# Kernel optimization log

Hardware: AMD Instinct MI355X
Metric: run time of the kernel (lower is better)

## Reference

```python
import jax, jax.numpy as jnp
import numpy as np

EPS_NORM = 1e-5   # instance-norm epsilon (NormalizeLayer over spatial axes)
EPS_VAR = 1e-9    # floor used before sqrt, as in the original


def _instance_norm(x):
    # normalize over spatial axes (1,2), per batch & channel
    mean = jnp.mean(x, axis=(1, 2), keepdims=True)
    var = jnp.var(x, axis=(1, 2), keepdims=True)
    return (x - mean) * jax.lax.rsqrt(var + EPS_NORM)


def _aat(content, style, comb_c, comb_s):
    # content/style: (B,H,W,C); comb_*: (B,H,W,Cc)
    B, H, W, C = content.shape
    N = H * W
    norm_content = _instance_norm(content)
    q = _instance_norm(comb_c).reshape(B, N, -1)   # (B,N,Cc)
    k = _instance_norm(comb_s).reshape(B, N, -1)   # (B,N,Cc)
    v = style.reshape(B, N, C)                     # (B,N,C)
    scores = jnp.einsum('bnc,bmc->bnm', q, k)      # Q_T @ K
    A = jax.nn.softmax(scores, axis=-1)            # (B,N,N)
    M = jnp.einsum('bnm,bmc->bnc', A, v)           # weighted mean
    S2 = jnp.einsum('bnm,bmc->bnc', A, v * v) - M * M  # weighted variance
    S = jnp.sqrt(jnp.maximum(jax.nn.relu(S2), EPS_VAR))
    S = S.reshape(B, H, W, C)
    M = M.reshape(B, H, W, C)
    return S * norm_content + M


def _feature_loss(cs, c, s, cc, sc):
    aat = _aat(c, s, cc, sc)
    return jnp.mean(jnp.square(cs - aat))


def setup_inputs() -> dict:
    key = jax.random.key(0)
    shapes = {
        'cs2': (4, 64, 64, 256), 'c2': (4, 64, 64, 256), 's2': (4, 64, 64, 256),
        'cc2': (4, 64, 64, 448), 'sc2': (4, 64, 64, 448),
        'cs3': (4, 32, 32, 512), 'c3': (4, 32, 32, 512), 's3': (4, 32, 32, 512),
        'cc3': (4, 32, 32, 960), 'sc3': (4, 32, 32, 960),
        'cs4': (4, 16, 16, 512), 'c4': (4, 16, 16, 512), 's4': (4, 16, 16, 512),
        'cc4': (4, 16, 16, 1472), 'sc4': (4, 16, 16, 1472),
    }
    keys = jax.random.split(key, len(shapes))
    return {name: jax.random.normal(k, shp, dtype=jnp.float32)
            for k, (name, shp) in zip(keys, shapes.items())}


def reference(cs2, c2, s2, cc2, sc2, cs3, c3, s3, cc3, sc3, cs4, c4, s4, cc4, sc4):
    loss = _feature_loss(cs2, c2, s2, cc2, sc2)
    loss = loss + _feature_loss(cs3, c3, s3, cc3, sc3)
    loss = loss + _feature_loss(cs4, c4, s4, cc4, sc4)
    return loss
```

## Files before the change

### kernel.cpp

```cpp
#include <hip/hip_runtime.h>
#include <math.h>

#define EPS_NORM 1e-5f
#define EPS_VAR  1e-9f
#define LOG2E    1.4426950408889634f

typedef unsigned short ushort_t;
typedef __attribute__((ext_vector_type(4))) float f32x4;
typedef _Float16 half8 __attribute__((ext_vector_type(8)));

#define MFMAH(a, b, c) __builtin_amdgcn_mfma_f32_16x16x32_f16((a), (b), (c), 0, 0, 0)

#define GLD16(gp, lp) __builtin_amdgcn_global_load_lds(                          \
    (const __attribute__((address_space(1))) unsigned int*)(gp),                 \
    (__attribute__((address_space(3))) unsigned int*)(lp), 16, 0, 0)

__device__ inline ushort_t f16_bits(float x) {
    _Float16 h = (_Float16)x;
    ushort_t u;
    __builtin_memcpy(&u, &h, 2);
    return u;
}
__device__ inline half8 ldh(const ushort_t* p) {
    half8 h;
    __builtin_memcpy(&h, p, 16);
    return h;
}
__device__ inline uint4 pack8(const ushort_t* s) {
    uint4 r;
    r.x = (unsigned)s[0] | ((unsigned)s[1] << 16);
    r.y = (unsigned)s[2] | ((unsigned)s[3] << 16);
    r.z = (unsigned)s[4] | ((unsigned)s[5] << 16);
    r.w = (unsigned)s[6] | ((unsigned)s[7] << 16);
    return r;
}

struct StatJobs {
    const float* x[9];
    float* sm[9];
    float* sq[9];
    int N[9], Cn[9], chG[9], nG[9], base[9];
};
__global__ void __launch_bounds__(256) stat_partial_all(StatJobs J)
{
    int bx = blockIdx.x;
    int j = 0;
#pragma unroll
    for (int k = 1; k < 9; ++k) if (bx >= J.base[k]) j = k;
    bx -= J.base[j];
    const int N = J.N[j], Cn = J.Cn[j], chG = J.chG[j], nG = J.nG[j];
    int b  = bx / (chG * nG);
    int r  = bx % (chG * nG);
    int cg = r / nG;
    int ng = r % nG;
    int ch = cg * 256 + threadIdx.x;
    if (ch >= Cn) return;
    int n0 = ng * 256;
    int n1 = min(n0 + 256, N);
    const float* p = J.x[j] + (long)(b * N) * Cn + ch;
    float s = 0.f, ss = 0.f;
    for (int n = n0; n < n1; ++n) {
        float v = p[(long)n * Cn];
        s += v;
        ss = fmaf(v, v, ss);
    }
    atomicAdd(&J.sm[j][b * Cn + ch], s);
    atomicAdd(&J.sq[j][b * Cn + ch], ss);
}

struct FinJobs {
    float* sm[9];
    float* sq[9];
    int base[9];
    float invN[9];
    int total;
};
__global__ void __launch_bounds__(256) stat_finalize_all(FinJobs J)
{
    int i = blockIdx.x * 256 + threadIdx.x;
    if (i >= J.total) return;
    int j = 0;
#pragma unroll
    for (int k = 1; k < 9; ++k) if (i >= J.base[k]) j = k;
    int e = i - J.base[j];
    float m = J.sm[j][e] * J.invN[j];
    float v = J.sq[j][e] * J.invN[j] - m * m;
    J.sm[j][e] = m;
    J.sq[j][e] = rsqrtf(v + EPS_NORM);
}

struct PrepJobs {
    const float* qx[3]; const float* qm[3]; const float* qr[3]; ushort_t* qh[3];
    const float* kx[3]; const float* km[3]; const float* kr[3]; ushort_t* kh[3];
    const float* vx[3]; ushort_t* vt[3];
    int N[3], Cc[3], C[3], nbase[3];
};
__global__ void __launch_bounds__(256) prep_all(PrepJobs J)
{
    __shared__ __align__(16) ushort_t tbuf[64 * 72];
    int bx = blockIdx.x;
    int j = 0;
#pragma unroll
    for (int k = 1; k < 3; ++k) if (bx >= J.nbase[k]) j = k;
    bx -= J.nbase[j];
    const int N = J.N[j], Cc = J.Cc[j];
    const int normBlocks = 2 * N;
    if (bx < normBlocks) {
        const int wave = threadIdx.x >> 6, lane = threadIdx.x & 63;
        int rr = bx * 4 + wave;
        const int BN = 4 * N;
        const bool isQ = rr < BN;
        int bn = isQ ? rr : rr - BN;
        const float* x    = isQ ? J.qx[j] : J.kx[j];
        const float* mean = isQ ? J.qm[j] : J.km[j];
        const float* rstd = isQ ? J.qr[j] : J.kr[j];
        ushort_t* out     = isQ ? J.qh[j] : J.kh[j];
        const float scl   = isQ ? LOG2E : 1.0f;
        int b = bn / N;
        long base = (long)bn * Cc;
        const float* mb = mean + b * Cc;
        const float* rb = rstd + b * Cc;
        for (int c8 = lane; c8 * 8 < Cc; c8 += 64) {
            int ch = c8 * 8;
            float4 a0 = *(const float4*)(x + base + ch);
            float4 a1 = *(const float4*)(x + base + ch + 4);
            float4 m0 = *(const float4*)(mb + ch);
            float4 m1 = *(const float4*)(mb + ch + 4);
            float4 r0 = *(const float4*)(rb + ch);
            float4 r1 = *(const float4*)(rb + ch + 4);
            ushort_t h8[8];
            h8[0] = f16_bits((a0.x - m0.x) * r0.x * scl);
            h8[1] = f16_bits((a0.y - m0.y) * r0.y * scl);
            h8[2] = f16_bits((a0.z - m0.z) * r0.z * scl);
            h8[3] = f16_bits((a0.w - m0.w) * r0.w * scl);
            h8[4] = f16_bits((a1.x - m1.x) * r1.x * scl);
            h8[5] = f16_bits((a1.y - m1.y) * r1.y * scl);
            h8[6] = f16_bits((a1.z - m1.z) * r1.z * scl);
            h8[7] = f16_bits((a1.w - m1.w) * r1.w * scl);
            *(uint4*)(out + base + ch) = pack8(h8);
        }
    } else {
        int bid2 = bx - normBlocks;
        const int C = J.C[j];
        const int cT = C >> 6, nT = N >> 6;
        int b   = bid2 / (cT * nT);
        int rem = bid2 % (cT * nT);
        int ch0 = (rem / nT) << 6;
        int n0  = (rem % nT) << 6;
        const int lane = threadIdx.x & 63, wv = threadIdx.x >> 6;
        const float* vb_ = J.vx[j] + (long)b * N * C + ch0 + lane;
#pragma unroll
        for (int jj = 0; jj < 2; ++jj) {
            int nl = wv * 16 + jj * 8;
            ushort_t h8[8];
#pragma unroll
            for (int i = 0; i < 8; ++i)
                h8[i] = f16_bits(vb_[(long)(n0 + nl + i) * C]);
            *(uint4*)&tbuf[lane * 72 + nl] = pack8(h8);
        }
        __syncthreads();
        {
            const int chl = threadIdx.x >> 2;
            const int nq  = (threadIdx.x & 3) * 16;
            ushort_t* op = J.vt[j] + ((long)b * C + ch0 + chl) * N + n0 + nq;
            *(uint4*)op       = *(const uint4*)&tbuf[chl * 72 + nq];
            *(uint4*)(op + 8) = *(const uint4*)&tbuf[chl * 72 + nq + 8];
        }
    }
}

__device__ inline void stage64_async(const ushort_t* __restrict__ g, long rowBase,
                                     int gstride, int col0, ushort_t* slab, int tid)
{
    const int l  = tid & 63, w = tid >> 6;
    const int rs = l >> 3;
    const int cg = (l & 7) ^ rs;
#pragma unroll
    for (int i = 0; i < 2; ++i) {
        const int r = w * 16 + i * 8 + rs;
        const ushort_t* gp = g + (rowBase + r) * (long)gstride + col0 + (cg << 3);
        ushort_t* lp = slab + (w * 16 + i * 8) * 64 + l * 8;
        GLD16(gp, lp);
    }
}
template<int BROWS>
__device__ inline void stageQ_async(const ushort_t* __restrict__ g, long rowBase,
                                    int gstride, int col0, ushort_t* slab, int tid)
{
    if (tid < BROWS * 8) {
        const int l  = tid & 63, w = tid >> 6;
        const int rs = l >> 3;
        const int cg = (l & 7) ^ rs;
        const int r  = w * 8 + rs;
        const ushort_t* gp = g + (rowBase + r) * (long)gstride + col0 + (cg << 3);
        ushort_t* lp = slab + w * 8 * 64 + l * 8;
        GLD16(gp, lp);
    }
}
__device__ inline half8 ldsw(const ushort_t* slab, int row, int soff)
{
    const int gr = (soff >> 3) ^ (row & 7);
    return ldh(slab + row * 64 + (gr << 3));
}

__global__ void __launch_bounds__(256, 2) flash_pipe(
    const ushort_t* __restrict__ Qh, const ushort_t* __restrict__ Kh,
    const ushort_t* __restrict__ Vth,
    float* __restrict__ Pmo, float* __restrict__ Plo,
    float* __restrict__ PMo, float* __restrict__ PSo)
{
    constexpr int Cc = 448, C = 256, N = 4096, SPLIT = 2;
    constexpr int NKT  = (N / 64) / SPLIT;
    constexpr long VCHO = 64L * N;
    constexpr long KADV = 64L * Cc;

    __shared__ __align__(16) ushort_t smem[4 * 8192 + 4 * 1152];
    const int tid  = threadIdx.x;
    const int lane = tid & 63;
    const int w    = tid >> 6;
    const int l15  = lane & 15;
    const int quad = lane >> 4;

    const int grp = blockIdx.x & 7;
    const int sp  = grp & 1;
    const int b   = grp >> 1;
    const int qb  = (int)(blockIdx.x >> 3);
    const int i0 = qb * 64 + w * 16;
    const long po = (long)(b * (N / 16) + qb * 4 + w) * SPLIT + sp;

    const int rs    = lane >> 3;
    const int cg    = (lane & 7) ^ rs;
    const int ldso0 = w * 1024 + lane * 8;
    const int ldso1 = ldso0 + 512;
    const int xh    = l15 & 7;
    const int lb0   = l15 * 64 + ((quad)     ^ xh) * 8;
    const int lb1   = l15 * 64 + ((4 + quad) ^ xh) * 8;
    ushort_t* const Pw  = smem + 32768 + w * 1152;
    ushort_t* const pww = Pw + quad * 288 + l15;
    const ushort_t* const pfr = Pw + l15 * 72 + quad * 8;

    const long krow0 = (long)b * N + (long)sp * NKT * 64;
    const ushort_t* kp0 = Kh + (krow0 + w * 16 + rs) * (long)Cc + (cg << 3);
    const ushort_t* kp1 = kp0 + 8 * Cc;
    const ushort_t* vp0 = Vth + ((long)b * C + w * 16 + rs) * (long)N
                              + (cg << 3) + (long)sp * NKT * 64;
    const ushort_t* vp1 = vp0 + 8 * (long)N;

#define SLOT(k) (smem + (k) * 8192)
#define STGKP(c0, c1, slot, toff) do {                                           \
    GLD16(kp0 + (toff) + (c0) * 64, SLOT(slot) + ldso0);                         \
    GLD16(kp1 + (toff) + (c0) * 64, SLOT(slot) + ldso1);                         \
    GLD16(kp0 + (toff) + (c1) * 64, SLOT(slot) + 4096 + ldso0);                  \
    GLD16(kp1 + (toff) + (c1) * 64, SLOT(slot) + 4096 + ldso1); } while (0)
#define STGK1(c0, slot, toff) do {                                               \
    GLD16(kp0 + (toff) + (c0) * 64, SLOT(slot) + ldso0);                         \
    GLD16(kp1 + (toff) + (c0) * 64, SLOT(slot) + ldso1); } while (0)
#define STGVP(j0, slot, voff) do {                                               \
    GLD16(vp0 + (voff) + (j0) * VCHO, SLOT(slot) + ldso0);                       \
    GLD16(vp1 + (voff) + (j0) * VCHO, SLOT(slot) + ldso1);                       \
    GLD16(vp0 + (voff) + ((j0) + 1) * VCHO, SLOT(slot) + 4096 + ldso0);          \
    GLD16(vp1 + (voff) + ((j0) + 1) * VCHO, SLOT(slot) + 4096 + ldso1); } while (0)

#define WAITV(NN) asm volatile("s_waitcnt vmcnt(" #NN ")" ::: "memory");         \
    __builtin_amdgcn_sched_barrier(0);                                           \
    __builtin_amdgcn_s_barrier();                                                \
    __builtin_amdgcn_s_setprio(1);
#define PH_END __builtin_amdgcn_s_setprio(0);

#define QKPAIR(slot, c0) do {                                                    \
    const ushort_t* s0_ = SLOT(slot);                                            \
    const ushort_t* s1_ = s0_ + 4096;                                            \
    _Pragma("unroll")                                                            \
    for (int ct = 0; ct < 4; ++ct) S[ct] = MFMAH(qf[2*(c0)+0], ldh(s0_ + ct*1024 + lb0), S[ct]); \
    _Pragma("unroll")                                                            \
    for (int ct = 0; ct < 4; ++ct) S[ct] = MFMAH(qf[2*(c0)+1], ldh(s0_ + ct*1024 + lb1), S[ct]); \
    _Pragma("unroll")                                                            \
    for (int ct = 0; ct < 4; ++ct) S[ct] = MFMAH(qf[2*(c0)+2], ldh(s1_ + ct*1024 + lb0), S[ct]); \
    _Pragma("unroll")                                                            \
    for (int ct = 0; ct < 4; ++ct) S[ct] = MFMAH(qf[2*(c0)+3], ldh(s1_ + ct*1024 + lb1), S[ct]); } while (0)
#define QK1(slot, c0) do {                                                       \
    const ushort_t* s0_ = SLOT(slot);                                            \
    _Pragma("unroll")                                                            \
    for (int ct = 0; ct < 4; ++ct) S[ct] = MFMAH(qf[2*(c0)+0], ldh(s0_ + ct*1024 + lb0), S[ct]); \
    _Pragma("unroll")                                                            \
    for (int ct = 0; ct < 4; ++ct) S[ct] = MFMAH(qf[2*(c0)+1], ldh(s0_ + ct*1024 + lb1), S[ct]); } while (0)
#define PVPAIR(slot, ci0) do {                                                   \
    const ushort_t* s0_ = SLOT(slot);                                            \
    const ushort_t* s1_ = s0_ + 4096;                                            \
    _Pragma("unroll")                                                            \
    for (int ct = 0; ct < 4; ++ct) {                                             \
        half8 vh = ldh(s0_ + ct*1024 + lb0); half8 uh = vh * vh;                 \
        Mac[(ci0)*4 + ct] = MFMAH(pf0, vh, Mac[(ci0)*4 + ct]);                   \
        Sac[(ci0)*4 + ct] = MFMAH(pf0, uh, Sac[(ci0)*4 + ct]); }                 \
    _Pragma("unroll")                                                            \
    for (int ct = 0; ct < 4; ++ct) {                                             \
        half8 vh = ldh(s0_ + ct*1024 + lb1); half8 uh = vh * vh;                 \
        Mac[(ci0)*4 + ct] = MFMAH(pf1, vh, Mac[(ci0)*4 + ct]);                   \
        Sac[(ci0)*4 + ct] = MFMAH(pf1, uh, Sac[(ci0)*4 + ct]); }                 \
    _Pragma("unroll")                                                            \
    for (int ct = 0; ct < 4; ++ct) {                                             \
        half8 vh = ldh(s1_ + ct*1024 + lb0); half8 uh = vh * vh;                 \
        Mac[(ci0+1)*4 + ct] = MFMAH(pf0, vh, Mac[(ci0+1)*4 + ct]);               \
        Sac[(ci0+1)*4 + ct] = MFMAH(pf0, uh, Sac[(ci0+1)*4 + ct]); }             \
    _Pragma("unroll")                                                            \
    for (int ct = 0; ct < 4; ++ct) {                                             \
        half8 vh = ldh(s1_ + ct*1024 + lb1); half8 uh = vh * vh;                 \
        Mac[(ci0+1)*4 + ct] = MFMAH(pf1, vh, Mac[(ci0+1)*4 + ct]);               \
        Sac[(ci0+1)*4 + ct] = MFMAH(pf1, uh, Sac[(ci0+1)*4 + ct]); } } while (0)
#define RESET_S do {                                                             \
    _Pragma("unroll")                                                            \
    for (int ct = 0; ct < 4; ++ct)                                               \
        _Pragma("unroll")                                                        \
        for (int r = 0; r < 4; ++r) S[ct][r] = 0.f; } while (0)

    half8 qf[14];
    {
        const ushort_t* q1 = Qh + ((long)(b * N + i0 + l15)) * Cc + quad * 8;
#pragma unroll
        for (int ks = 0; ks < 14; ++ks) qf[ks] = ldh(q1 + ks * 32);
    }
    asm volatile("s_waitcnt vmcnt(0)" ::: "memory");

    float m_r[4], l_l[4], mw = -1e30f;
    f32x4 Mac[16], Sac[16];
    f32x4 S[4];
    half8 pf0, pf1;
#pragma unroll
    for (int r = 0; r < 4; ++r) { m_r[r] = -1e30f; l_l[r] = 0.f; }
#pragma unroll
    for (int ct = 0; ct < 16; ++ct)
#pragma unroll
        for (int r = 0; r < 4; ++r) { Mac[ct][r] = 0.f; Sac[ct][r] = 0.f; }

    auto softmax_step = [&]() {
        float tmax = S[0][0];
#pragma unroll
        for (int ct = 0; ct < 4; ++ct)
#pragma unroll
            for (int r = 0; r < 4; ++r) tmax = fmaxf(tmax, S[ct][r]);
#pragma unroll
        for (int off = 1; off <= 32; off <<= 1)
            tmax = fmaxf(tmax, __shfl_xor(tmax, off, 64));

        if (tmax > mw + 14.4269504f) {
            float rm[4];
#pragma unroll
            for (int r = 0; r < 4; ++r)
                rm[r] = fmaxf(fmaxf(S[0][r], S[1][r]), fmaxf(S[2][r], S[3][r]));
#pragma unroll
            for (int off = 1; off <= 8; off <<= 1)
#pragma unroll
                for (int r = 0; r < 4; ++r)
                    rm[r] = fmaxf(rm[r], __shfl_xor(rm[r], off, 64));
#pragma unroll
            for (int r = 0; r < 4; ++r) {
                float mn = fmaxf(m_r[r], rm[r]);
                float corr = exp2f(m_r[r] - mn);
                m_r[r] = mn;
                l_l[r] *= corr;
#pragma unroll
                for (int ct = 0; ct < 16; ++ct) { Mac[ct][r] *= corr; Sac[ct][r] *= corr; }
            }
            float tt = fminf(fminf(m_r[0], m_r[1]), fminf(m_r[2], m_r[3]));
            tt = fminf(tt, __shfl_xor(tt, 16, 64));
            tt = fminf(tt, __shfl_xor(tt, 32, 64));
            mw = tt;
        }
#pragma unroll
        for (int ct = 0; ct < 4; ++ct)
#pragma unroll
            for (int r = 0; r < 4; ++r) {
                float p = exp2f(S[ct][r] - m_r[r]);
                l_l[r] += p;
                pww[r * 72 + ct * 16] = f16_bits(p);
            }
        pf0 = ldh(pfr);
        pf1 = ldh(pfr + 32);
    };

    STGKP(0, 1, 0, 0);
    STGKP(2, 3, 1, 0);

    for (int it = 0; it < NKT / 2; ++it) {
        RESET_S;
        STGKP(4, 5, 2, 0);
        WAITV(8)  QKPAIR(0, 0); PH_END;
        STGK1(6, 3, 0);
        WAITV(6)  QKPAIR(1, 2); PH_END;
        STGVP(0, 0, 0);
        WAITV(6)  QKPAIR(2, 4); PH_END;
        STGVP(2, 1, 0);
        WAITV(8)  QK1(3, 6); PH_END;
        softmax_step();
        STGKP(0, 1, 2, KADV);
        WAITV(8)  PVPAIR(0, 0); PH_END;
        STGKP(2, 3, 3, KADV);
        WAITV(8)  PVPAIR(1, 2); PH_END;

        RESET_S;
        STGKP(4, 5, 0, KADV);
        WAITV(8)  QKPAIR(2, 0); PH_END;
        STGK1(6, 1, KADV);
        WAITV(6)  QKPAIR(3, 2); PH_END;
        STGVP(0, 2, 64);
        WAITV(6)  QKPAIR(0, 4); PH_END;
        STGVP(2, 3, 64);
        WAITV(8)  QK1(1, 6); PH_END;
        softmax_step();
        const bool more = (it + 1 < NKT / 2);
        if (more) {
            kp0 += 2 * KADV; kp1 += 2 * KADV;
            STGKP(0, 1, 0, 0);
            asm volatile("s_waitcnt vmcnt(8)" ::: "memory");
        } else {
            asm volatile("s_waitcnt vmcnt(4)" ::: "memory");
        }
        __builtin_amdgcn_sched_barrier(0);
        __builtin_amdgcn_s_barrier();
        __builtin_amdgcn_s_setprio(1);
        PVPAIR(2, 0);
        PH_END;
        if (more) {
            STGKP(2, 3, 1, 0);
            asm volatile("s_waitcnt vmcnt(8)" ::: "memory");
        } else {
            asm volatile("s_waitcnt vmcnt(0)" ::: "memory");
        }
        __builtin_amdgcn_sched_barrier(0);
        __builtin_amdgcn_s_barrier();
        __builtin_amdgcn_s_setprio(1);
        PVPAIR(3, 2);
        PH_END;

        vp0 += 128; vp1 += 128;
    }
#undef SLOT
#undef STGKP
#undef STGK1
#undef STGVP
#undef WAITV
#undef PH_END
#undef QKPAIR
#undef QK1
#undef PVPAIR
#undef RESET_S

#pragma unroll
    for (int off = 1; off <= 8; off <<= 1)
#pragma unroll
        for (int r = 0; r < 4; ++r) l_l[r] += __shfl_xor(l_l[r], off, 64);

    if (l15 == 0) {
#pragma unroll
        for (int r = 0; r < 4; ++r) {
            Pmo[po * 16 + quad * 4 + r] = m_r[r];
            Plo[po * 16 + quad * 4 + r] = l_l[r];
        }
    }
#pragma unroll
    for (int ct = 0; ct < 16; ++ct)
#pragma unroll
        for (int r = 0; r < 4; ++r) {
            long idx = (po * 16 + quad * 4 + r) * C + ct * 16 + l15;
            PMo[idx] = Mac[ct][r];
            PSo[idx] = Sac[ct][r];
        }
}

template<int Cc, int C, int N, int CSPLIT, bool QREG, int SPLIT, int SLABS, int KGRP>
__global__ void __launch_bounds__(256, 2) flash_mfma(
    const ushort_t* __restrict__ Qh, const ushort_t* __restrict__ Kh,
    const ushort_t* __restrict__ Vth,
    float* __restrict__ Pmo, float* __restrict__ Plo,
    float* __restrict__ PMo, float* __restrict__ PSo)
{
    constexpr int KC      = Cc / 64;
    constexpr int VC      = C / 64;
    constexpr int VCW     = VC / CSPLIT;
    constexpr int CTCW    = 4 * VCW;
    constexpr int STRIPES = 4 / CSPLIT;
    constexpr int BROWS   = 16 * STRIPES;
    constexpr int QB      = N / BROWS;
    constexpr int TILES   = N / 64;
    constexpr int NKT     = TILES / SPLIT;
    constexpr int NKS     = QREG ? (Cc / 32) : 1;
    constexpr int NGRP    = (KC + KGRP - 1) / KGRP;
    constexpr int G       = 4 / CSPLIT;
    constexpr int QCH     = BROWS * 64;
    constexpr int QOFF    = KGRP * 4096;
    constexpr int KQEND   = QOFF + KGRP * QCH;
    constexpr int REGION  = QREG ? (SLABS * 4096)
                                 : (KQEND > SLABS * 4096 ? KQEND : SLABS * 4096);

    __shared__ __align__(16) ushort_t smem[REGION + 4 * 1152];
    const int tid  = threadIdx.x;
    const int lane = tid & 63;
    const int w    = tid >> 6;
    const int l15  = lane & 15;
    const int quad = lane >> 4;

    const int bq = blockIdx.x / SPLIT;
    const int sp = blockIdx.x % SPLIT;
    const int b  = bq / QB;
    const int qb = bq % QB;
    const int ls  = w / CSPLIT;
    const int ch2 = w % CSPLIT;
    const int i0 = qb * BROWS + ls * 16;
    const long po = (long)(b * (N / 16) + qb * STRIPES + ls) * SPLIT + sp;
    ushort_t* Pw = smem + REGION + w * 1152;

    half8 qf[NKS];
    if constexpr (QREG) {
        const ushort_t* q1 = Qh + ((long)(b * N + i0 + l15)) * Cc + quad * 8;
#pragma unroll
        for (int ks = 0; ks < NKS; ++ks) qf[ks] = ldh(q1 + ks * 32);
    }

    float m_r[4], l_l[4], mw = -1e30f;
    f32x4 Mac[CTCW], Sac[CTCW];
#pragma unroll
    for (int r = 0; r < 4; ++r) { m_r[r] = -1e30f; l_l[r] = 0.f; }
#pragma unroll
    for (int ct = 0; ct < CTCW; ++ct)
#pragma unroll
        for (int r = 0; r < 4; ++r) { Mac[ct][r] = 0.f; Sac[ct][r] = 0.f; }

    for (int kt = sp * NKT; kt < sp * NKT + NKT; ++kt) {
        const long krow = (long)b * N + kt * 64;

        f32x4 S[4];
#pragma unroll
        for (int ct = 0; ct < 4; ++ct)
#pragma unroll
            for (int r = 0; r < 4; ++r) S[ct][r] = 0.f;

#pragma unroll
        for (int grp = 0; grp < NGRP; ++grp) {
            const int g0 = grp * KGRP;
            const int gn = (KC - g0 < KGRP) ? (KC - g0) : KGRP;
            __syncthreads();
#pragma unroll
            for (int j = 0; j < KGRP; ++j) if (j < gn) {
                stage64_async(Kh, krow, Cc, (g0 + j) * 64, smem + j * 4096, tid);
                if constexpr (!QREG)
                    stageQ_async<BROWS>(Qh, (long)b * N + qb * BROWS, Cc, (g0 + j) * 64,
                                        smem + QOFF + j * QCH, tid);
            }
            __syncthreads();
#pragma unroll
            for (int j = 0; j < KGRP; ++j) if (j < gn) {
#pragma unroll
                for (int ks = 0; ks < 2; ++ks) {
                    half8 a;
                    if constexpr (QREG) a = qf[(g0 + j) * 2 + ks];
                    else a = ldsw(smem + QOFF + j * QCH, ls * 16 + l15, ks * 32 + quad * 8);
#pragma unroll
                    for (int ct = 0; ct < 4; ++ct) {
                        half8 bf = ldsw(smem + j * 4096, ct * 16 + l15, ks * 32 + quad * 8);
                        S[ct] = MFMAH(a, bf, S[ct]);
                    }
                }
            }
        }

        float tmax = S[0][0];
#pragma unroll
        for (int ct = 0; ct < 4; ++ct)
#pragma unroll
            for (int r = 0; r < 4; ++r) tmax = fmaxf(tmax, S[ct][r]);
#pragma unroll
        for (int off = 1; off <= 32; off <<= 1)
            tmax = fmaxf(tmax, __shfl_xor(tmax, off, 64));

        if (tmax > mw + 14.4269504f) {
            float rm[4];
#pragma unroll
            for (int r = 0; r < 4; ++r)
                rm[r] = fmaxf(fmaxf(S[0][r], S[1][r]), fmaxf(S[2][r], S[3][r]));
#pragma unroll
            for (int off = 1; off <= 8; off <<= 1)
#pragma unroll
                for (int r = 0; r < 4; ++r)
                    rm[r] = fmaxf(rm[r], __shfl_xor(rm[r], off, 64));
#pragma unroll
            for (int r = 0; r < 4; ++r) {
                float mn = fmaxf(m_r[r], rm[r]);
                float corr = exp2f(m_r[r] - mn);
                m_r[r] = mn;
                l_l[r] *= corr;
#pragma unroll
                for (int ct = 0; ct < CTCW; ++ct) { Mac[ct][r] *= corr; Sac[ct][r] *= corr; }
            }
            float t = fminf(fminf(m_r[0], m_r[1]), fminf(m_r[2], m_r[3]));
            t = fminf(t, __shfl_xor(t, 16, 64));
            t = fminf(t, __shfl_xor(t, 32, 64));
            mw = t;
        }

#pragma unroll
        for (int ct = 0; ct < 4; ++ct)
#pragma unroll
            for (int r = 0; r < 4; ++r) {
                float p = exp2f(S[ct][r] - m_r[r]);
                l_l[r] += p;
                Pw[(quad * 4 + r) * 72 + ct * 16 + l15] = f16_bits(p);
            }

        half8 pf0 = ldh(Pw + l15 * 72 + 0  + quad * 8);
        half8 pf1 = ldh(Pw + l15 * 72 + 32 + quad * 8);

#pragma unroll
        for (int g = 0; g < VCW; g += G) {
            __syncthreads();
#pragma unroll
            for (int s = 0; s < 4; ++s) {
                const int h = s / G, j = s % G;
                stage64_async(Vth, (long)b * C + (h * VCW + g + j) * 64, N, kt * 64,
                              smem + s * 4096, tid);
            }
            __syncthreads();
#pragma unroll
            for (int ks = 0; ks < 2; ++ks) {
                half8 pf = ks ? pf1 : pf0;
#pragma unroll
                for (int j = 0; j < G; ++j)
#pragma unroll
                    for (int ct = 0; ct < 4; ++ct) {
                        half8 vh = ldsw(smem + (ch2 * G + j) * 4096,
                                        ct * 16 + l15, ks * 32 + quad * 8);
                        half8 uh = vh * vh;
                        const int ci = (g + j) * 4 + ct;
                        Mac[ci] = MFMAH(pf, vh, Mac[ci]);
                        Sac[ci] = MFMAH(pf, uh, Sac[ci]);
                    }
            }
        }
    }

#pragma unroll
    for (int off = 1; off <= 8; off <<= 1)
#pragma unroll
        for (int r = 0; r < 4; ++r) l_l[r] += __shfl_xor(l_l[r], off, 64);

    if (ch2 == 0 && l15 == 0) {
#pragma unroll
        for (int r = 0; r < 4; ++r) {
            Pmo[po * 16 + quad * 4 + r] = m_r[r];
            Plo[po * 16 + quad * 4 + r] = l_l[r];
        }
    }
    const int chb = ch2 * (C / CSPLIT);
#pragma unroll
    for (int ct = 0; ct < CTCW; ++ct)
#pragma unroll
        for (int r = 0; r < 4; ++r) {
            long idx = (po * 16 + quad * 4 + r) * C + chb + ct * 16 + l15;
            PMo[idx] = Mac[ct][r];
            PSo[idx] = Sac[ct][r];
        }
}

template<int C, int SPLIT>
__global__ void __launch_bounds__(256) combine_aat(
    const float* __restrict__ Pm, const float* __restrict__ Pl,
    const float* __restrict__ PM, const float* __restrict__ PS,
    const float* __restrict__ CT, const float* __restrict__ CS,
    const float* __restrict__ cmean, const float* __restrict__ crstd,
    float* __restrict__ loss, int N)
{
    constexpr int CL4 = C / 4;
    __shared__ float wS[SPLIT][16];
    __shared__ float invL[16];
    __shared__ float red[4];
    const int pi = blockIdx.x;
    const int nb = N / 16;
    const int b  = pi / nb;
    const long g0 = (long)b * N + (long)(pi % nb) * 16;
    const int tid = threadIdx.x;

    if (tid < 16) {
        float m = -1e30f;
#pragma unroll
        for (int s = 0; s < SPLIT; ++s)
            m = fmaxf(m, Pm[((long)pi * SPLIT + s) * 16 + tid]);
        float L = 0.f;
#pragma unroll
        for (int s = 0; s < SPLIT; ++s) {
            float e = exp2f(Pm[((long)pi * SPLIT + s) * 16 + tid] - m);
            wS[s][tid] = e;
            L = fmaf(e, Pl[((long)pi * SPLIT + s) * 16 + tid], L);
        }
        invL[tid] = 1.f / L;
    }
    __syncthreads();

    float acc = 0.f;
    for (int v = tid; v < 4 * C; v += 256) {
        const int r  = v / CL4;
        const int c0 = (v - r * CL4) * 4;
        const long q0 = (((long)pi * SPLIT) * 16 + r) * C + c0;
        float4 Ms = {0.f, 0.f, 0.f, 0.f}, Ss = {0.f, 0.f, 0.f, 0.f};
#pragma unroll
        for (int s = 0; s < SPLIT; ++s) {
            const float ws_ = wS[s][r];
            const float4 pm = *(const float4*)&PM[q0 + (long)s * 16 * C];
            const float4 ps = *(const float4*)&PS[q0 + (long)s * 16 * C];
            Ms.x = fmaf(ws_, pm.x, Ms.x); Ms.y = fmaf(ws_, pm.y, Ms.y);
            Ms.z = fmaf(ws_, pm.z, Ms.z); Ms.w = fmaf(ws_, pm.w, Ms.w);
            Ss.x = fmaf(ws_, ps.x, Ss.x); Ss.y = fmaf(ws_, ps.y, Ss.y);
            Ss.z = fmaf(ws_, ps.z, Ss.z); Ss.w = fmaf(ws_, ps.w, Ss.w);
        }
        const float iL = invL[r];
        const float4 ctv = *(const float4*)&CT[(g0 + r) * C + c0];
        const float4 csv = *(const float4*)&CS[(g0 + r) * C + c0];
        const float4 cmv = *(const float4*)&cmean[b * C + c0];
        const float4 crv = *(const float4*)&crstd[b * C + c0];
#pragma unroll
        for (int e = 0; e < 4; ++e) {
            const float Msx = (&Ms.x)[e] * iL;
            const float S2  = (&Ss.x)[e] * iL - Msx * Msx;
            const float Sx  = sqrtf(fmaxf(S2, EPS_VAR));
            const float nc  = ((&ctv.x)[e] - (&cmv.x)[e]) * (&crv.x)[e];
            const float d   = (&csv.x)[e] - (Sx * nc + Msx);
            acc = fmaf(d, d, acc);
        }
    }
#pragma unroll
    for (int off = 1; off <= 32; off <<= 1) acc += __shfl_xor(acc, off, 64);
    if ((tid & 63) == 0) red[tid >> 6] = acc;
    __syncthreads();
    if (tid == 0) atomicAdd(loss, red[0] + red[1] + red[2] + red[3]);
}

template<int CCL, int CL, int NQ>
__global__ void __launch_bounds__(256) flash_aat(
    const float* __restrict__ Q, const float* __restrict__ K, const float* __restrict__ V,
    const float* __restrict__ CT, const float* __restrict__ CS,
    const float* __restrict__ qmean, const float* __restrict__ qrstd,
    const float* __restrict__ kmean, const float* __restrict__ krstd,
    const float* __restrict__ cmean, const float* __restrict__ crstd,
    float* __restrict__ loss, int N)
{
    constexpr int CC   = CCL * 64;
    constexpr int C    = CL * 64;
    constexpr int ROWS = 4 * NQ;
    const int lane = threadIdx.x & 63;
    const int wave = threadIdx.x >> 6;
    const int rowBlocks = N / ROWS;
    const int b  = blockIdx.x / rowBlocks;
    const int rb = blockIdx.x % rowBlocks;
    const int i0 = rb * ROWS + wave * NQ;

    float kmu[CCL], krs[CCL];
#pragma unroll
    for (int t = 0; t < CCL; ++t) {
        int ch = lane + 64 * t;
        kmu[t] = kmean[b * CC + ch];
        krs[t] = krstd[b * CC + ch];
    }
    float q[NQ][CCL];
#pragma unroll
    for (int qi = 0; qi < NQ; ++qi) {
        long base = (long)(b * N + i0 + qi) * CC;
#pragma unroll
        for (int t = 0; t < CCL; ++t) {
            int ch = lane + 64 * t;
            q[qi][t] = (Q[base + ch] - qmean[b * CC + ch]) * qrstd[b * CC + ch];
        }
    }
    float mval[NQ], lsum[NQ];
    float Macc[NQ][CL], Sacc[NQ][CL];
#pragma unroll
    for (int qi = 0; qi < NQ; ++qi) {
        mval[qi] = -1e30f; lsum[qi] = 0.f;
#pragma unroll
        for (int t = 0; t < CL; ++t) { Macc[qi][t] = 0.f; Sacc[qi][t] = 0.f; }
    }
    for (int j = 0; j < N; ++j) {
        long kb = (long)(b * N + j) * CC;
        float dot[NQ];
#pragma unroll
        for (int qi = 0; qi < NQ; ++qi) dot[qi] = 0.f;
#pragma unroll
        for (int t = 0; t < CCL; ++t) {
            float kv = (K[kb + lane + 64 * t] - kmu[t]) * krs[t];
#pragma unroll
            for (int qi = 0; qi < NQ; ++qi) dot[qi] = fmaf(q[qi][t], kv, dot[qi]);
        }
#pragma unroll
        for (int off = 32; off > 0; off >>= 1)
#pragma unroll
            for (int qi = 0; qi < NQ; ++qi) dot[qi] += __shfl_xor(dot[qi], off, 64);
        long vb = (long)(b * N + j) * C;
        float vv[CL];
#pragma unroll
        for (int t = 0; t < CL; ++t) vv[t] = V[vb + lane + 64 * t];
#pragma unroll
        for (int qi = 0; qi < NQ; ++qi) {
            float s = dot[qi];
            float p;
            if (s > mval[qi]) {
                float cr2 = __expf(mval[qi] - s);
                lsum[qi] *= cr2;
#pragma unroll
                for (int t = 0; t < CL; ++t) { Macc[qi][t] *= cr2; Sacc[qi][t] *= cr2; }
                mval[qi] = s; p = 1.f;
            } else p = __expf(s - mval[qi]);
            lsum[qi] += p;
#pragma unroll
            for (int t = 0; t < CL; ++t) {
                float pv = p * vv[t];
                Macc[qi][t] += pv;
                Sacc[qi][t] = fmaf(pv, vv[t], Sacc[qi][t]);
            }
        }
    }
    float acc = 0.f;
#pragma unroll
    for (int qi = 0; qi < NQ; ++qi) {
        float inv_l = 1.f / lsum[qi];
        long base = (long)(b * N + i0 + qi) * C;
#pragma unroll
        for (int t = 0; t < CL; ++t) {
            int ch = lane + 64 * t;
            float M  = Macc[qi][t] * inv_l;
            float S2 = Sacc[qi][t] * inv_l - M * M;
            float S  = sqrtf(fmaxf(S2, EPS_VAR));
            float nc = (CT[base + ch] - cmean[b * C + ch]) * crstd[b * C + ch];
            float d  = CS[base + ch] - (S * nc + M);
            acc = fmaf(d, d, acc);
        }
    }
#pragma unroll
    for (int off = 32; off > 0; off >>= 1) acc += __shfl_xor(acc, off, 64);
    if (lane == 0) atomicAdd(loss, acc);
}

__global__ void combine_loss(const float* __restrict__ lp, float* __restrict__ out,
                             float s0, float s1, float s2)
{
    out[0] = lp[0] * s0 + lp[1] * s1 + lp[2] * s2;
}

extern "C" void kernel_launch(void* const* d_in, const int* in_sizes, int n_in,
                              void* d_out, int out_size, void* d_ws, size_t ws_size,
                              hipStream_t stream)
{
    const float* cs2 = (const float*)d_in[0];
    const float* c2  = (const float*)d_in[1];
    const float* s2v = (const float*)d_in[2];
    const float* cc2 = (const float*)d_in[3];
    const float* sc2 = (const float*)d_in[4];
    const float* cs3 = (const float*)d_in[5];
    const float* c3  = (const float*)d_in[6];
    const float* s3v = (const float*)d_in[7];
    const float* cc3 = (const float*)d_in[8];
    const float* sc3 = (const float*)d_in[9];
    const float* cs4 = (const float*)d_in[10];
    const float* c4  = (const float*)d_in[11];
    const float* s4v = (const float*)d_in[12];
    const float* cc4 = (const float*)d_in[13];
    const float* sc4 = (const float*)d_in[14];

    const int B = 4;
    float* ws = (float*)d_ws;
    size_t fo = 0;
    auto allocF = [&](size_t n) { float* p = ws + fo; fo += n; return p; };

    float* lossp = allocF(4);
    float* c2m = allocF(B * 256);  float* c2r = allocF(B * 256);
    float* q2m = allocF(B * 448);  float* q2r = allocF(B * 448);
    float* k2m = allocF(B * 448);  float* k2r = allocF(B * 448);
    float* c3m = allocF(B * 512);  float* c3r = allocF(B * 512);
    float* q3m = allocF(B * 960);  float* q3r = allocF(B * 960);
    float* k3m = allocF(B * 960);  float* k3r = allocF(B * 960);
    float* c4m = allocF(B * 512);  float* c4r = allocF(B * 512);
    float* q4m = allocF(B * 1472); float* q4r = allocF(B * 1472);
    float* k4m = allocF(B * 1472); float* k4r = allocF(B * 1472);
    size_t zeroBytes = fo * sizeof(float);

    float* Pm = allocF(32768);
    float* Pl = allocF(32768);
    float* PM = allocF(8388608);
    float* PS = allocF(8388608);

    size_t arenaOff = ((fo * 4 + 15) & ~(size_t)15) / 2;
    ushort_t* arena = (ushort_t*)d_ws + arenaOff;
    const size_t arenaShorts = 18874400;
    size_t need = arenaOff * 2 + arenaShorts * 2;
    const bool fast = (ws_size >= need);

    hipMemsetAsync(d_ws, 0, zeroBytes, stream);

    {
        StatJobs SJ; FinJobs FJ;
        const float* xs[9] = {c2, cc2, sc2, c3, cc3, sc3, c4, cc4, sc4};
        float* sms[9] = {c2m, q2m, k2m, c3m, q3m, k3m, c4m, q4m, k4m};
        float* sqs[9] = {c2r, q2r, k2r, c3r, q3r, k3r, c4r, q4r, k4r};
        const int Ns[9]  = {4096, 4096, 4096, 1024, 1024, 1024, 256, 256, 256};
        const int Cns[9] = {256, 448, 448, 512, 960, 960, 512, 1472, 1472};
        int pb = 0, fb = 0;
        for (int j = 0; j < 9; ++j) {
            int chG = (Cns[j] + 255) / 256;
            int nG  = (Ns[j] + 255) / 256;
            SJ.x[j] = xs[j]; SJ.sm[j] = sms[j]; SJ.sq[j] = sqs[j];
            SJ.N[j] = Ns[j]; SJ.Cn[j] = Cns[j]; SJ.chG[j] = chG; SJ.nG[j] = nG;
            SJ.base[j] = pb;
            pb += B * chG * nG;
            FJ.sm[j] = sms[j]; FJ.sq[j] = sqs[j]; FJ.base[j] = fb;
            FJ.invN[j] = 1.0f / (float)Ns[j];
            fb += B * Cns[j];
        }
        FJ.total = fb;
        hipLaunchKernelGGL(stat_partial_all, dim3(pb), dim3(256), 0, stream, SJ);
        hipLaunchKernelGGL(stat_finalize_all, dim3((fb + 255) / 256), dim3(256), 0, stream, FJ);
    }

    if (fast) {
        auto arenaFor = [&](size_t& o, size_t n) {
            ushort_t* p = arena + o; o += (n + 7) & ~(size_t)7; return p;
        };
        size_t o2 = 0;
        ushort_t* qh2 = arenaFor(o2, (size_t)B*4096*448);
        ushort_t* kh2 = arenaFor(o2, (size_t)B*4096*448);
        ushort_t* vh2 = arenaFor(o2, (size_t)B*4096*256);
        size_t o3 = 0;
        ushort_t* qh3 = arenaFor(o3, (size_t)B*1024*960);
        ushort_t* kh3 = arenaFor(o3, (size_t)B*1024*960);
        ushort_t* vh3 = arenaFor(o3, (size_t)B*1024*512);
        size_t o4 = 0;
        ushort_t* qh4 = arenaFor(o4, (size_t)B*256*1472);
        ushort_t* kh4 = arenaFor(o4, (size_t)B*256*1472);
        ushort_t* vh4 = arenaFor(o4, (size_t)B*256*512);

        const int vt2 = (256/64)*(4096/64)*B;
        const int vt3 = (512/64)*(1024/64)*B;
        const int vt4 = (512/64)*(256/64)*B;

        size_t totShorts = o2 + o3 + o4;
        bool prepFused = (ws_size >= arenaOff * 2 + totShorts * 2);
        if (prepFused) {
            qh3 = arena + o2;        kh3 = qh3 + (((size_t)B*1024*960 + 7) & ~(size_t)7);
            vh3 = kh3 + (((size_t)B*1024*960 + 7) & ~(size_t)7);
            qh4 = arena + o2 + o3;   kh4 = qh4 + (((size_t)B*256*1472 + 7) & ~(size_t)7);
            vh4 = kh4 + (((size_t)B*256*1472 + 7) & ~(size_t)7);

            PrepJobs PJ;
            PJ.qx[0]=cc2; PJ.qm[0]=q2m; PJ.qr[0]=q2r; PJ.qh[0]=qh2;
            PJ.kx[0]=sc2; PJ.km[0]=k2m; PJ.kr[0]=k2r; PJ.kh[0]=kh2;
            PJ.vx[0]=s2v; PJ.vt[0]=vh2; PJ.N[0]=4096; PJ.Cc[0]=448; PJ.C[0]=256;
            PJ.qx[1]=cc3; PJ.qm[1]=q3m; PJ.qr[1]=q3r; PJ.qh[1]=qh3;
            PJ.kx[1]=sc3; PJ.km[1]=k3m; PJ.kr[1]=k3r; PJ.kh[1]=kh3;
            PJ.vx[1]=s3v; PJ.vt[1]=vh3; PJ.N[1]=1024; PJ.Cc[1]=960; PJ.C[1]=512;
            PJ.qx[2]=cc4; PJ.qm[2]=q4m; PJ.qr[2]=q4r; PJ.qh[2]=qh4;
            PJ.kx[2]=sc4; PJ.km[2]=k4m; PJ.kr[2]=k4r; PJ.kh[2]=kh4;
            PJ.vx[2]=s4v; PJ.vt[2]=vh4; PJ.N[2]=256;  PJ.Cc[2]=1472; PJ.C[2]=512;
            int g0n = 2*4096 + vt2;
            int g1n = 2*1024 + vt3;
            int g2n = 2*256  + vt4;
            PJ.nbase[0] = 0; PJ.nbase[1] = g0n; PJ.nbase[2] = g0n + g1n;
            hipLaunchKernelGGL(prep_all, dim3(g0n + g1n + g2n), dim3(256), 0, stream, PJ);
        }

        {
            if (!prepFused) {
                PrepJobs PJ;
                PJ.qx[0]=cc2; PJ.qm[0]=q2m; PJ.qr[0]=q2r; PJ.qh[0]=qh2;
                PJ.kx[0]=sc2; PJ.km[0]=k2m; PJ.kr[0]=k2r; PJ.kh[0]=kh2;
                PJ.vx[0]=s2v; PJ.vt[0]=vh2; PJ.N[0]=4096; PJ.Cc[0]=448; PJ.C[0]=256;
                for (int k = 1; k < 3; ++k) { PJ.N[k]=4096; PJ.Cc[k]=448; PJ.C[k]=256;
                    PJ.qx[k]=cc2; PJ.qm[k]=q2m; PJ.qr[k]=q2r; PJ.qh[k]=qh2;
                    PJ.kx[k]=sc2; PJ.km[k]=k2m; PJ.kr[k]=k2r; PJ.kh[k]=kh2;
                    PJ.vx[k]=s2v; PJ.vt[k]=vh2; }
                int gn = 2*4096 + vt2;
                PJ.nbase[0]=0; PJ.nbase[1]=gn; PJ.nbase[2]=gn;
                hipLaunchKernelGGL(prep_all, dim3(gn), dim3(256), 0, stream, PJ);
            }
            hipLaunchKernelGGL(flash_pipe, dim3(B*(4096/64)*2), dim3(256), 0, stream,
                               qh2, kh2, vh2, Pm, Pl, PM, PS);
            hipLaunchKernelGGL((combine_aat<256, 2>), dim3(B*4096/16), dim3(256), 0, stream,
                               Pm, Pl, PM, PS, c2, cs2, c2m, c2r, &lossp[0], 4096);
        }
        {
            if (!prepFused) {
                PrepJobs PJ;
                PJ.qx[0]=cc3; PJ.qm[0]=q3m; PJ.qr[0]=q3r; PJ.qh[0]=qh3;
                PJ.kx[0]=sc3; PJ.km[0]=k3m; PJ.kr[0]=k3r; PJ.kh[0]=kh3;
                PJ.vx[0]=s3v; PJ.vt[0]=vh3; PJ.N[0]=1024; PJ.Cc[0]=960; PJ.C[0]=512;
                for (int k = 1; k < 3; ++k) { PJ.N[k]=1024; PJ.Cc[k]=960; PJ.C[k]=512;
                    PJ.qx[k]=cc3; PJ.qm[k]=q3m; PJ.qr[k]=q3r; PJ.qh[k]=qh3;
                    PJ.kx[k]=sc3; PJ.km[k]=k3m; PJ.kr[k]=k3r; PJ.kh[k]=kh3;
                    PJ.vx[k]=s3v; PJ.vt[k]=vh3; }
                int gn = 2*1024 + vt3;
                PJ.nbase[0]=0; PJ.nbase[1]=gn; PJ.nbase[2]=gn;
                hipLaunchKernelGGL(prep_all, dim3(gn), dim3(256), 0, stream, PJ);
            }
            hipLaunchKernelGGL((flash_mfma<960, 512, 1024, 2, false, 4, 5, 5>),
                               dim3(B*(1024/32)*4), dim3(256), 0, stream,
                               qh3, kh3, vh3, Pm, Pl, PM, PS);
            hipLaunchKernelGGL((combine_aat<512, 4>), dim3(B*1024/16), dim3(256), 0, stream,
                               Pm, Pl, PM, PS, c3, cs3, c3m, c3r, &lossp[1], 1024);
        }
        {
            if (!prepFused) {
                PrepJobs PJ;
                PJ.qx[0]=cc4; PJ.qm[0]=q4m; PJ.qr[0]=q4r; PJ.qh[0]=qh4;
                PJ.kx[0]=sc4; PJ.km[0]=k4m; PJ.kr[0]=k4r; PJ.kh[0]=kh4;
                PJ.vx[0]=s4v; PJ.vt[0]=vh4; PJ.N[0]=256; PJ.Cc[0]=1472; PJ.C[0]=512;
                for (int k = 1; k < 3; ++k) { PJ.N[k]=256; PJ.Cc[k]=1472; PJ.C[k]=512;
                    PJ.qx[k]=cc4; PJ.qm[k]=q4m; PJ.qr[k]=q4r; PJ.qh[k]=qh4;
                    PJ.kx[k]=sc4; PJ.km[k]=k4m; PJ.kr[k]=k4r; PJ.kh[k]=kh4;
                    PJ.vx[k]=s4v; PJ.vt[k]=vh4; }
                int gn = 2*256 + vt4;
                PJ.nbase[0]=0; PJ.nbase[1]=gn; PJ.nbase[2]=gn;
                hipLaunchKernelGGL(prep_all, dim3(gn), dim3(256), 0, stream, PJ);
            }
            hipLaunchKernelGGL((flash_mfma<1472, 512, 256, 4, false, 4, 6, 6>),
                               dim3(B*(256/16)*4), dim3(256), 0, stream,
                               qh4, kh4, vh4, Pm, Pl, PM, PS);
            hipLaunchKernelGGL((combine_aat<512, 4>), dim3(B*256/16), dim3(256), 0, stream,
                               Pm, Pl, PM, PS, c4, cs4, c4m, c4r, &lossp[2], 256);
        }
    } else {
        hipLaunchKernelGGL((flash_aat<7, 4, 4>), dim3(B * 4096 / 16), dim3(256), 0, stream,
                           cc2, sc2, s2v, c2, cs2, q2m, q2r, k2m, k2r, c2m, c2r, &lossp[0], 4096);
        hipLaunchKernelGGL((flash_aat<15, 8, 2>), dim3(B * 1024 / 8), dim3(256), 0, stream,
                           cc3, sc3, s3v, c3, cs3, q3m, q3r, k3m, k3r, c3m, c3r, &lossp[1], 1024);
        hipLaunchKernelGGL((flash_aat<23, 8, 2>), dim3(B * 256 / 8), dim3(256), 0, stream,
                           cc4, sc4, s4v, c4, cs4, q4m, q4r, k4m, k4r, c4m, c4r, &lossp[2], 256);
    }

    hipLaunchKernelGGL(combine_loss, dim3(1), dim3(1), 0, stream,
                       lossp, (float*)d_out,
                       1.0f / (4.0f * 4096.0f * 256.0f),
                       1.0f / (4.0f * 1024.0f * 512.0f),
                       1.0f / (4.0f * 256.0f * 512.0f));
}
```

Baseline: 682.1 us.

## Fuse level-3 and level-4 flash/combine launches and split QK^T across channel waves

Merges the level-3 and level-4 flash kernels into one grid, and likewise their combine kernels, so the smaller level-4 work fills the GPU alongside level 3 instead of running as a separate underfilled launch. Inside flash_body, waves that share a row stripe but handle different output-channel halves now each compute only a subset of the Cc chunks of Q·K^T and sum partial scores through shared memory, removing the redundant score MFMAs those waves used to repeat. Level-4 partials go to a separate workspace tail. The cost is two extra block barriers per key tile plus LDS traffic for the reduction, and a fixed shared-memory size across both instantiations.

```diff
diff --git a/kernel.cpp b/kernel.cpp
--- a/kernel.cpp
+++ b/kernel.cpp
@@ -468,11 +468,12 @@
 }
 
 template<int Cc, int C, int N, int CSPLIT, bool QREG, int SPLIT, int SLABS, int KGRP>
-__global__ void __launch_bounds__(256, 2) flash_mfma(
+__device__ __forceinline__ void flash_body(
     const ushort_t* __restrict__ Qh, const ushort_t* __restrict__ Kh,
     const ushort_t* __restrict__ Vth,
     float* __restrict__ Pmo, float* __restrict__ Plo,
-    float* __restrict__ PMo, float* __restrict__ PSo)
+    float* __restrict__ PMo, float* __restrict__ PSo,
+    ushort_t* smem, int bid)
 {
     constexpr int KC      = Cc / 64;
     constexpr int VC      = C / 64;
@@ -492,15 +493,14 @@
     constexpr int REGION  = QREG ? (SLABS * 4096)
                                  : (KQEND > SLABS * 4096 ? KQEND : SLABS * 4096);
 
-    __shared__ __align__(16) ushort_t smem[REGION + 4 * 1152];
     const int tid  = threadIdx.x;
     const int lane = tid & 63;
     const int w    = tid >> 6;
     const int l15  = lane & 15;
     const int quad = lane >> 4;
 
-    const int bq = blockIdx.x / SPLIT;
-    const int sp = blockIdx.x % SPLIT;
+    const int bq = bid / SPLIT;
+    const int sp = bid % SPLIT;
     const int b  = bq / QB;
     const int qb = bq % QB;
     const int ls  = w / CSPLIT;
@@ -549,16 +549,37 @@
             __syncthreads();
 #pragma unroll
             for (int j = 0; j < KGRP; ++j) if (j < gn) {
-#pragma unroll
-                for (int ks = 0; ks < 2; ++ks) {
-                    half8 a;
-                    if constexpr (QREG) a = qf[(g0 + j) * 2 + ks];
-                    else a = ldsw(smem + QOFF + j * QCH, ls * 16 + l15, ks * 32 + quad * 8);
-#pragma unroll
-                    for (int ct = 0; ct < 4; ++ct) {
-                        half8 bf = ldsw(smem + j * 4096, ct * 16 + l15, ks * 32 + quad * 8);
-                        S[ct] = MFMAH(a, bf, S[ct]);
+                if (((g0 + j) % CSPLIT) == ch2) {
+#pragma unroll
+                    for (int ks = 0; ks < 2; ++ks) {
+                        half8 a;
+                        if constexpr (QREG) a = qf[(g0 + j) * 2 + ks];
+                        else a = ldsw(smem + QOFF + j * QCH, ls * 16 + l15, ks * 32 + quad * 8);
+#pragma unroll
+                        for (int ct = 0; ct < 4; ++ct) {
+                            half8 bf = ldsw(smem + j * 4096, ct * 16 + l15, ks * 32 + quad * 8);
+                            S[ct] = MFMAH(a, bf, S[ct]);
+                        }
                     }
+                }
+            }
+        }
+
+        if constexpr (CSPLIT > 1) {
+            float* sred = (float*)smem;
+            __syncthreads();
+#pragma unroll
+            for (int ct = 0; ct < 4; ++ct)
+                *(f32x4*)&sred[(w * 4 + ct) * 256 + lane * 4] = S[ct];
+            __syncthreads();
+#pragma unroll
+            for (int p = 0; p < 4; ++p) {
+                if (p == w) continue;
+                if ((p / CSPLIT) != ls) continue;
+#pragma unroll
+                for (int ct = 0; ct < 4; ++ct) {
+                    f32x4 t = *(const f32x4*)&sred[(p * 4 + ct) * 256 + lane * 4];
+                    S[ct] = S[ct] + t;
                 }
             }
         }
@@ -660,19 +681,49 @@
         }
 }
 
+template<int Cc, int C, int N, int CSPLIT, bool QREG, int SPLIT, int SLABS, int KGRP>
+__global__ void __launch_bounds__(256, 2) flash_mfma(
+    const ushort_t* __restrict__ Qh, const ushort_t* __restrict__ Kh,
+    const ushort_t* __restrict__ Vth,
+    float* __restrict__ Pmo, float* __restrict__ Plo,
+    float* __restrict__ PMo, float* __restrict__ PSo)
+{
+    __shared__ __align__(16) ushort_t smem[35328];
+    flash_body<Cc, C, N, CSPLIT, QREG, SPLIT, SLABS, KGRP>(
+        Qh, Kh, Vth, Pmo, Plo, PMo, PSo, smem, (int)blockIdx.x);
+}
+
+__global__ void __launch_bounds__(256, 2) flash34(
+    const ushort_t* __restrict__ Qh3, const ushort_t* __restrict__ Kh3,
+    const ushort_t* __restrict__ Vth3,
+    float* __restrict__ Pm3, float* __restrict__ Pl3,
+    float* __restrict__ PM3, float* __restrict__ PS3,
+    const ushort_t* __restrict__ Qh4, const ushort_t* __restrict__ Kh4,
+    const ushort_t* __restrict__ Vth4,
+    float* __restrict__ Pm4, float* __restrict__ Pl4,
+    float* __restrict__ PM4, float* __restrict__ PS4, int G3)
+{
+    __shared__ __align__(16) ushort_t smem[35328];
+    if ((int)blockIdx.x < G3)
+        flash_body<960, 512, 1024, 2, false, 4, 5, 5>(
+            Qh3, Kh3, Vth3, Pm3, Pl3, PM3, PS3, smem, (int)blockIdx.x);
+    else
+        flash_body<1472, 512, 256, 4, false, 4, 6, 6>(
+            Qh4, Kh4, Vth4, Pm4, Pl4, PM4, PS4, smem, (int)blockIdx.x - G3);
+}
+
 template<int C, int SPLIT>
-__global__ void __launch_bounds__(256) combine_aat(
+__device__ __forceinline__ void combine_body(
     const float* __restrict__ Pm, const float* __restrict__ Pl,
     const float* __restrict__ PM, const float* __restrict__ PS,
     const float* __restrict__ CT, const float* __restrict__ CS,
     const float* __restrict__ cmean, const float* __restrict__ crstd,
-    float* __restrict__ loss, int N)
+    float* __restrict__ loss, int N, int pi, float* shm)
 {
     constexpr int CL4 = C / 4;
-    __shared__ float wS[SPLIT][16];
-    __shared__ float invL[16];
-    __shared__ float red[4];
-    const int pi = blockIdx.x;
+    float (*wS)[16] = (float(*)[16])shm;
+    float* invL = shm + SPLIT * 16;
+    float* red  = invL + 16;
     const int nb = N / 16;
     const int b  = pi / nb;
     const long g0 = (long)b * N + (long)(pi % nb) * 16;
@@ -730,6 +781,40 @@
     if ((tid & 63) == 0) red[tid >> 6] = acc;
     __syncthreads();
     if (tid == 0) atomicAdd(loss, red[0] + red[1] + red[2] + red[3]);
+}
+
+template<int C, int SPLIT>
+__global__ void __launch_bounds__(256) combine_aat(
+    const float* __restrict__ Pm, const float* __restrict__ Pl,
+    const float* __restrict__ PM, const float* __restrict__ PS,
+    const float* __restrict__ CT, const float* __restrict__ CS,
+    const float* __restrict__ cmean, const float* __restrict__ crstd,
+    float* __restrict__ loss, int N)
+{
+    __shared__ float shm[SPLIT * 16 + 20];
+    combine_body<C, SPLIT>(Pm, Pl, PM, PS, CT, CS, cmean, crstd, loss, N,
+                           (int)blockIdx.x, shm);
+}
+
+__global__ void __launch_bounds__(256) combine34(
+    const float* __restrict__ Pm3, const float* __restrict__ Pl3,
+    const float* __restrict__ PM3, const float* __restrict__ PS3,
+    const float* __restrict__ CT3, const float* __restrict__ CS3,
+    const float* __restrict__ cm3, const float* __restrict__ cr3,
+    float* __restrict__ l3, int N3,
+    const float* __restrict__ Pm4, const float* __restrict__ Pl4,
+    const float* __restrict__ PM4, const float* __restrict__ PS4,
+    const float* __restrict__ CT4, const float* __restrict__ CS4,
+    const float* __restrict__ cm4, const float* __restrict__ cr4,
+    float* __restrict__ l4, int N4, int G3)
+{
+    __shared__ float shm[4 * 16 + 20];
+    if ((int)blockIdx.x < G3)
+        combine_body<512, 4>(Pm3, Pl3, PM3, PS3, CT3, CS3, cm3, cr3, l3, N3,
+                             (int)blockIdx.x, shm);
+    else
+        combine_body<512, 4>(Pm4, Pl4, PM4, PS4, CT4, CS4, cm4, cr4, l4, N4,
+                             (int)blockIdx.x - G3, shm);
 }
 
 template<int CCL, int CL, int NQ>
@@ -939,6 +1024,16 @@
 
         size_t totShorts = o2 + o3 + o4;
         bool prepFused = (ws_size >= arenaOff * 2 + totShorts * 2);
+
+        const size_t PS4N = (size_t)256 * 16 * 512;
+        size_t tailByte = (((arenaOff + totShorts) * 2) + 255) & ~(size_t)255;
+        bool fused34 = prepFused && (ws_size >= tailByte + 2 * PS4N * 4);
+        float* PM4 = nullptr; float* PS4 = nullptr;
+        if (fused34) {
+            PM4 = (float*)((char*)d_ws + tailByte);
+            PS4 = PM4 + PS4N;
+        }
+
         if (prepFused) {
             qh3 = arena + o2;        kh3 = qh3 + (((size_t)B*1024*960 + 7) & ~(size_t)7);
             vh3 = kh3 + (((size_t)B*1024*960 + 7) & ~(size_t)7);
@@ -981,45 +1076,60 @@
             hipLaunchKernelGGL((combine_aat<256, 2>), dim3(B*4096/16), dim3(256), 0, stream,
                                Pm, Pl, PM, PS, c2, cs2, c2m, c2r, &lossp[0], 4096);
         }
-        {
-            if (!prepFused) {
-                PrepJobs PJ;
-                PJ.qx[0]=cc3; PJ.qm[0]=q3m; PJ.qr[0]=q3r; PJ.qh[0]=qh3;
-                PJ.kx[0]=sc3; PJ.km[0]=k3m; PJ.kr[0]=k3r; PJ.kh[0]=kh3;
-                PJ.vx[0]=s3v; PJ.vt[0]=vh3; PJ.N[0]=1024; PJ.Cc[0]=960; PJ.C[0]=512;
-                for (int k = 1; k < 3; ++k) { PJ.N[k]=1024; PJ.Cc[k]=960; PJ.C[k]=512;
-                    PJ.qx[k]=cc3; PJ.qm[k]=q3m; PJ.qr[k]=q3r; PJ.qh[k]=qh3;
-                    PJ.kx[k]=sc3; PJ.km[k]=k3m; PJ.kr[k]=k3r; PJ.kh[k]=kh3;
-                    PJ.vx[k]=s3v; PJ.vt[k]=vh3; }
-                int gn = 2*1024 + vt3;
-                PJ.nbase[0]=0; PJ.nbase[1]=gn; PJ.nbase[2]=gn;
-                hipLaunchKernelGGL(prep_all, dim3(gn), dim3(256), 0, stream, PJ);
-            }
-            hipLaunchKernelGGL((flash_mfma<960, 512, 1024, 2, false, 4, 5, 5>),
-                               dim3(B*(1024/32)*4), dim3(256), 0, stream,
-                               qh3, kh3, vh3, Pm, Pl, PM, PS);
-            hipLaunchKernelGGL((combine_aat<512, 4>), dim3(B*1024/16), dim3(256), 0, stream,
-                               Pm, Pl, PM, PS, c3, cs3, c3m, c3r, &lossp[1], 1024);
-        }
-        {
-            if (!prepFused) {
-                PrepJobs PJ;
-                PJ.qx[0]=cc4; PJ.qm[0]=q4m; PJ.qr[0]=q4r; PJ.qh[0]=qh4;
-                PJ.kx[0]=sc4; PJ.km[0]=k4m; PJ.kr[0]=k4r; PJ.kh[0]=kh4;
-                PJ.vx[0]=s4v; PJ.vt[0]=vh4; PJ.N[0]=256; PJ.Cc[0]=1472; PJ.C[0]=512;
-                for (int k = 1; k < 3; ++k) { PJ.N[k]=256; PJ.Cc[k]=1472; PJ.C[k]=512;
-                    PJ.qx[k]=cc4; PJ.qm[k]=q4m; PJ.qr[k]=q4r; PJ.qh[k]=qh4;
-                    PJ.kx[k]=sc4; PJ.km[k]=k4m; PJ.kr[k]=k4r; PJ.kh[k]=kh4;
-                    PJ.vx[k]=s4v; PJ.vt[k]=vh4; }
-                int gn = 2*256 + vt4;
-                PJ.nbase[0]=0; PJ.nbase[1]=gn; PJ.nbase[2]=gn;
-                hipLaunchKernelGGL(prep_all, dim3(gn), dim3(256), 0, stream, PJ);
-            }
-            hipLaunchKernelGGL((flash_mfma<1472, 512, 256, 4, false, 4, 6, 6>),
-                               dim3(B*(256/16)*4), dim3(256), 0, stream,
-                               qh4, kh4, vh4, Pm, Pl, PM, PS);
-            hipLaunchKernelGGL((combine_aat<512, 4>), dim3(B*256/16), dim3(256), 0, stream,
-                               Pm, Pl, PM, PS, c4, cs4, c4m, c4r, &lossp[2], 256);
+
+        if (fused34) {
+            const int G3 = B*(1024/32)*4;
+            const int G4 = B*(256/16)*4;
+            hipLaunchKernelGGL(flash34, dim3(G3 + G4), dim3(256), 0, stream,
+                               qh3, kh3, vh3, Pm, Pl, PM, PS,
+                               qh4, kh4, vh4, Pm + 16384, Pl + 16384, PM4, PS4, G3);
+            const int C3 = B*1024/16;
+            const int C4 = B*256/16;
+            hipLaunchKernelGGL(combine34, dim3(C3 + C4), dim3(256), 0, stream,
+                               Pm, Pl, PM, PS, c3, cs3, c3m, c3r, &lossp[1], 1024,
+                               Pm + 16384, Pl + 16384, PM4, PS4,
+                               c4, cs4, c4m, c4r, &lossp[2], 256, C3);
+        } else {
+            {
+                if (!prepFused) {
+                    PrepJobs PJ;
+                    PJ.qx[0]=cc3; PJ.qm[0]=q3m; PJ.qr[0]=q3r; PJ.qh[0]=qh3;
+                    PJ.kx[0]=sc3; PJ.km[0]=k3m; PJ.kr[0]=k3r; PJ.kh[0]=kh3;
+                    PJ.vx[0]=s3v; PJ.vt[0]=vh3; PJ.N[0]=1024; PJ.Cc[0]=960; PJ.C[0]=512;
+                    for (int k = 1; k < 3; ++k) { PJ.N[k]=1024; PJ.Cc[k]=960; PJ.C[k]=512;
+                        PJ.qx[k]=cc3; PJ.qm[k]=q3m; PJ.qr[k]=q3r; PJ.qh[k]=qh3;
+                        PJ.kx[k]=sc3; PJ.km[k]=k3m; PJ.kr[k]=k3r; PJ.kh[k]=kh3;
+                        PJ.vx[k]=s3v; PJ.vt[k]=vh3; }
+                    int gn = 2*1024 + vt3;
+                    PJ.nbase[0]=0; PJ.nbase[1]=gn; PJ.nbase[2]=gn;
+                    hipLaunchKernelGGL(prep_all, dim3(gn), dim3(256), 0, stream, PJ);
+                }
+                hipLaunchKernelGGL((flash_mfma<960, 512, 1024, 2, false, 4, 5, 5>),
+                                   dim3(B*(1024/32)*4), dim3(256), 0, stream,
+                                   qh3, kh3, vh3, Pm, Pl, PM, PS);
+                hipLaunchKernelGGL((combine_aat<512, 4>), dim3(B*1024/16), dim3(256), 0, stream,
+                                   Pm, Pl, PM, PS, c3, cs3, c3m, c3r, &lossp[1], 1024);
+            }
+            {
+                if (!prepFused) {
+                    PrepJobs PJ;
+                    PJ.qx[0]=cc4; PJ.qm[0]=q4m; PJ.qr[0]=q4r; PJ.qh[0]=qh4;
+                    PJ.kx[0]=sc4; PJ.km[0]=k4m; PJ.kr[0]=k4r; PJ.kh[0]=kh4;
+                    PJ.vx[0]=s4v; PJ.vt[0]=vh4; PJ.N[0]=256; PJ.Cc[0]=1472; PJ.C[0]=512;
+                    for (int k = 1; k < 3; ++k) { PJ.N[k]=256; PJ.Cc[k]=1472; PJ.C[k]=512;
+                        PJ.qx[k]=cc4; PJ.qm[k]=q4m; PJ.qr[k]=q4r; PJ.qh[k]=qh4;
+                        PJ.kx[k]=sc4; PJ.km[k]=k4m; PJ.kr[k]=k4r; PJ.kh[k]=kh4;
+                        PJ.vx[k]=s4v; PJ.vt[k]=vh4; }
+                    int gn = 2*256 + vt4;
+                    PJ.nbase[0]=0; PJ.nbase[1]=gn; PJ.nbase[2]=gn;
+                    hipLaunchKernelGGL(prep_all, dim3(gn), dim3(256), 0, stream, PJ);
+                }
+                hipLaunchKernelGGL((flash_mfma<1472, 512, 256, 4, false, 4, 6, 6>),
+                                   dim3(B*(256/16)*4), dim3(256), 0, stream,
+                                   qh4, kh4, vh4, Pm, Pl, PM, PS);
+                hipLaunchKernelGGL((combine_aat<512, 4>), dim3(B*256/16), dim3(256), 0, stream,
+                                   Pm, Pl, PM, PS, c4, cs4, c4m, c4r, &lossp[2], 256);
+            }
         }
     } else {
         hipLaunchKernelGGL((flash_aat<7, 4, 4>), dim3(B * 4096 / 16), dim3(256), 0, stream,
```

After: 672.4 us. Within noise of the previous version (-1.4%).
